# Optimization experiments

Measured on AMD Instinct MI355X. Metric: run time of the kernel, lower is better.

The kernel has to match this reference:

```python
import jax, jax.numpy as jnp
import numpy as np

N_HID = 256
N_IN = 2
N_OUT = 2
BATCH = 256
LENGTH = 1024
ALPHA = 0.25
SIGMA_NEU = 0.05
N_CON = 6553


def setup_inputs() -> dict:
    key = jax.random.key(0)
    k1, k2, k3, k4, k5 = jax.random.split(key, 5)
    rng = np.random.RandomState(0)
    # masked recurrent weight pieces (match torch __init__ construction)
    w_0 = rng.randn(N_HID, N_HID) / np.sqrt(N_HID)
    abs_w_0 = jnp.asarray(np.abs(w_0), dtype=jnp.float32)
    is_con_np = np.zeros((N_HID, N_HID), dtype=np.float32)
    ind_in = rng.choice(np.arange(N_HID), size=N_CON)
    ind_out = rng.choice(np.arange(N_HID), size=N_CON)
    is_con_np[ind_in, ind_out] = 1.0
    w_sign = jnp.asarray(np.sign(rng.randn(N_HID, N_HID)), dtype=jnp.float32)
    is_con = jnp.asarray(is_con_np)
    return {
        "input_signal": jax.random.normal(k1, (BATCH, LENGTH, N_IN), dtype=jnp.float32),
        "hidden": jnp.zeros((BATCH, N_HID), dtype=jnp.float32),
        "w_in": jax.random.normal(k2, (N_HID, N_IN), dtype=jnp.float32) / np.sqrt(N_IN),
        "w_out": jax.random.normal(k3, (N_OUT, N_HID), dtype=jnp.float32) / np.sqrt(N_HID),
        "abs_w_0": abs_w_0,
        "w_sign": w_sign,
        "is_con": is_con,
    }


def reference(input_signal, hidden, w_in, w_out, abs_w_0, w_sign, is_con):
    # masked signed recurrent weight: theta = |w0| * mask; w_hh = sign * theta where mask>0
    theta = abs_w_0 * is_con
    w_hh = jnp.where(is_con > 0, w_sign * theta, jnp.zeros_like(theta))  # [H,H]

    alpha = jnp.full((N_HID,), ALPHA, dtype=input_signal.dtype)
    x = jnp.transpose(input_signal, (1, 0, 2))  # [T,B,I]
    # input projection for all timesteps at once (w_in has no bias)
    inp_proj = jnp.einsum("tbi,hi->tbh", x, w_in)  # [T,B,H]
    # iid per-step neural noise: randn * sigma * sqrt(alpha)
    noise = (jax.random.normal(jax.random.key(42), (LENGTH, BATCH, N_HID), dtype=input_signal.dtype)
             * SIGMA_NEU * jnp.sqrt(alpha))

    def step(h, uv):
        u, n = uv
        tmp = u + jnp.tanh(h) @ w_hh.T  # F.linear(tanh(h), w_hh)
        h_new = (1.0 - alpha) * h + alpha * tmp + n
        return h_new, h_new

    h_last, hs = jax.lax.scan(step, hidden, (inp_proj, noise))  # hs: [T,B,H]
    outputs = jnp.einsum("tbh,oh->tbo", hs, w_out)  # [T,B,O]
    hidden_list = jnp.transpose(hs, (1, 0, 2))  # [B,T,H]
    output_list = jnp.transpose(outputs, (1, 0, 2))  # [B,T,O]
    return hidden_list, output_list, h_last
```

## Files before the change

### kernel.cpp

```cpp
#include <hip/hip_runtime.h>
#include <stdint.h>

#define TT 1024
#define HB 256
#define NE 48
#define NE2 24
#define O1 67108864u
#define O2 (67108864u + 524288u)

__device__ __forceinline__ uint32_t rotl32(uint32_t x, uint32_t r){ return (x<<r)|(x>>(32u-r)); }

#define RND(r) { x0+=x1; x1=rotl32(x1,(r)); x1^=x0; }
__device__ __forceinline__ void tf2x32(uint32_t k0,uint32_t k1,uint32_t& x0,uint32_t& x1){
  const uint32_t ks2 = 0x1BD11BDAu ^ k0 ^ k1;
  x0 += k0; x1 += k1;
  RND(13) RND(15) RND(26) RND(6)  x0+=k1;  x1+=ks2+1u;
  RND(17) RND(29) RND(16) RND(24) x0+=ks2; x1+=k0+2u;
  RND(13) RND(15) RND(26) RND(6)  x0+=k0;  x1+=k1+3u;
  RND(17) RND(29) RND(16) RND(24) x0+=k1;  x1+=ks2+4u;
  RND(13) RND(15) RND(26) RND(6)  x0+=ks2; x1+=k0+5u;
}
#undef RND

__device__ __forceinline__ float bits_to_noise(uint32_t bits){
  float f = __uint_as_float((bits>>9) | 0x3F800000u) - 1.0f;
  const float lo = -0.99999994f;
  float x = fmaxf(fmaf(f, 1.99999994f, lo), lo);
  float m = (1.0f - x) * (1.0f + x);
  float w = -0.69314718056f * __log2f(m);
  float p;
  if (w < 5.0f){
    w -= 2.5f;
    p = 2.81022636e-08f;
    p = fmaf(p, w, 3.43273939e-07f);
    p = fmaf(p, w, -3.5233877e-06f);
    p = fmaf(p, w, -4.39150654e-06f);
    p = fmaf(p, w, 0.00021858087f);
    p = fmaf(p, w, -0.00125372503f);
    p = fmaf(p, w, -0.00417768164f);
    p = fmaf(p, w, 0.246640727f);
    p = fmaf(p, w, 1.50140941f);
  } else {
    w = __fsqrt_rn(w) - 3.0f;
    p = -0.000200214257f;
    p = fmaf(p, w, 0.000100950558f);
    p = fmaf(p, w, 0.00134934322f);
    p = fmaf(p, w, -0.00367342844f);
    p = fmaf(p, w, 0.00573950773f);
    p = fmaf(p, w, -0.0076224613f);
    p = fmaf(p, w, 0.00943887047f);
    p = fmaf(p, w, 1.00167406f);
    p = fmaf(p, w, 2.83297682f);
  }
  return 0.035355339059f * (p * x);
}

__global__ void init_flags(uint32_t* flags){
  if (flags) { flags[0]=0u; flags[1]=0u; }
}

__global__ void check_kernel(float* out, const uint32_t* flags){
  uint32_t a0=0u, a1=0u;                 tf2x32(0u,0u,a0,a1);
  uint32_t b0=0xffffffffu, b1=0xffffffffu; tf2x32(0xffffffffu,0xffffffffu,b0,b1);
  uint32_t c0=0x243f6a88u, c1=0x85a308d3u; tf2x32(0x13198a2eu,0x03707344u,c0,c1);
  if (!(a0==0x6b200159u && a1==0x99ba4efeu)) out[0] = 1e30f;
  if (!(b0==0x1cb996fcu && b1==0xbb002be7u)) out[1] = 2e30f;
  if (!(c0==0xc4923a9cu && c1==0x483df7a0u)) out[2] = 3e30f;
  if (flags && flags[0]) out[5] = 6e30f;
}

__launch_bounds__(1024)
__global__ void rnn_kernel(const float* __restrict__ input_signal,
                           const float* __restrict__ hidden0,
                           const float* __restrict__ w_in,
                           const float* __restrict__ w_out,
                           const float* __restrict__ abs_w0,
                           const float* __restrict__ w_sign,
                           const float* __restrict__ is_con,
                           float* __restrict__ out,
                           uint32_t* __restrict__ flags)
{
  __shared__ float    ew[HB][NE];
  __shared__ uint16_t ei[HB][NE];
  __shared__ float    xbuf[TT*2];
  __shared__ float    hstage[8][HB];
  __shared__ float    nbuf[4][HB];
  __shared__ float    tbuf[2][HB];
  __shared__ int      cnts[HB];
  __shared__ int      rankinv[HB];
  __shared__ int      rof4[HB];
  __shared__ float    wot0[HB], wot1[HB];

  const int tid = threadIdx.x;
  const int b   = blockIdx.x;
  const bool gw = (tid < 512);

  {
    const float* xg = input_signal + (uint64_t)b*TT*2;
    *(float2*)(xbuf + tid*2) = *(const float2*)(xg + tid*2);
  }
  if (tid < HB){
    int c = 0;
    const float* ic = is_con + tid*HB;
    for (int k = 0; k < HB; k += 4){
      float4 c4 = *(const float4*)(ic + k);
      c += (c4.x>0.f)+(c4.y>0.f)+(c4.z>0.f)+(c4.w>0.f);
    }
    cnts[tid] = c;
    if (c > NE && flags) flags[0] = 1u;
  }
  __syncthreads();

  if (tid < HB){
    int myc = cnts[tid], r = 0;
    for (int k = 0; k < HB; ++k){
      int ck = cnts[k];
      r += (int)((ck > myc) || (ck == myc && k < tid));
    }
    rankinv[r] = tid;
    rof4[tid]  = r << 2;
  }
  __syncthreads();

  uint32_t bj = 0u;
  if (tid < HB){
    const int j = tid;
    const float* ic = is_con + j*HB;
    const float* aw = abs_w0 + j*HB;
    const float* ws = w_sign + j*HB;
    int n = 0;
    for (int k = 0; k < HB; ++k){
      if (ic[k] > 0.f && n < NE){
        ew[j][n] = ws[k]*aw[k];
        ei[j][n] = (uint16_t)rof4[k];
        ++n;
      }
    }
    for (int s = n; s < NE; ++s){ ew[j][s] = 0.f; ei[j][s] = (uint16_t)rof4[j]; }
    wot0[rof4[j]>>2] = w_out[j];
    wot1[rof4[j]>>2] = w_out[HB + j];
  } else if (tid >= 512){
    int m = tid - 512, rn = m >> 1, qn = m & 1;
    bj = (uint32_t)b*256u + (uint32_t)rankinv[rn];
    if (qn == 0){
      uint32_t x0 = 0u, x1 = bj;
      tf2x32(0u, 42u, x0, x1);
      nbuf[0][rn] = bits_to_noise(x0 ^ x1);
    }
  }
  __syncthreads();

  float    pwv[NE2];
  uint32_t piv[NE2/2];
  int trip = 0, row = 0, q = 0, rr = 0;
  float h = 0.f, wi0 = 0.f, wi1 = 0.f;
  float4 wo0 = {0,0,0,0}, wo1 = {0,0,0,0};
  int rf0 = 0, rf1 = 0;
  {
    int j0 = (tid & 127) << 1;
    rf0 = rof4[j0]; rf1 = rof4[j0+1];
  }
  if (gw){
    rr = tid >> 1; q = tid & 1;
    row = rankinv[rr];
    int c = cnts[row]; if (c > NE) c = NE;
    uint16_t pad = (uint16_t)rof4[row];
    uint32_t cur = 0u;
    #pragma unroll
    for (int s = 0; s < NE2; ++s){
      int idx = 2*s + q;
      float w = 0.f; uint32_t o = pad;
      if (idx < c){ w = ew[row][idx]; o = ei[row][idx]; }
      pwv[s] = w;
      if (s & 1) piv[s>>1] = cur | (o << 16); else cur = o;
    }
    trip = __builtin_amdgcn_readfirstlane((c + 1) >> 1);
    if (q == 0){
      h   = hidden0[b*HB + row];
      wi0 = w_in[row*2]; wi1 = w_in[row*2 + 1];
      tbuf[0][rr] = 1.0f - 2.0f/(__expf(2.0f*h) + 1.0f);
    }
  } else {
    int m = tid - 512;
    if (m < 128){
      int lam = m & 63;
      wo0 = *(const float4*)(wot0 + lam*4);
      wo1 = *(const float4*)(wot1 + lam*4);
    }
  }
  float* hrow = out + (uint64_t)b*TT*HB;
  float* orow = out + O1 + (uint64_t)b*TT*2;
  __syncthreads();

  for (int t = 0; t < TT; ++t){
    const int par = t & 1;
    if (gw){
      const char* tb = (const char*)(&tbuf[par][0]);
      float y0 = 0.f, y1 = 0.f;
      #pragma unroll
      for (int s = 0; s < NE2; s += 2){
        if (s < trip){
          uint32_t pa = piv[s>>1];
          float t0 = *(const float*)(tb + (pa & 0xFFFFu));
          float t1 = *(const float*)(tb + (pa >> 16));
          y0 = fmaf(pwv[s],   t0, y0);
          y1 = fmaf(pwv[s+1], t1, y1);
        }
      }
      float y = y0 + y1;
      y += __shfl_xor(y, 1, 64);
      if (q == 0){
        float nz = nbuf[t&3][rr];
        float2 xv = *(const float2*)(xbuf + t*2);
        float u  = fmaf(xv.x, wi0, xv.y*wi1);
        h = fmaf(0.25f, u + y, 0.75f*h) + nz;
        hstage[t&7][rr] = h;
        tbuf[par^1][rr] = 1.0f - 2.0f/(__expf(2.0f*h) + 1.0f);
      }
    } else {
      int m = tid - 512;
      if (!(t & 1)){
        int tv = t + 1 + (m & 1);
        if (tv < TT){
          uint32_t x0 = 0u, x1 = (uint32_t)tv*65536u + bj;
          tf2x32(0u, 42u, x0, x1);
          nbuf[tv&3][m>>1] = bits_to_noise(x0 ^ x1);
        }
      } else if (m < 128){
        int tau = t - 2 + (m >> 6);
        if (tau >= 0){
          int lam = m & 63;
          float4 hv = *(const float4*)(&hstage[tau&7][lam*4]);
          float p0 = hv.x*wo0.x + hv.y*wo0.y + hv.z*wo0.z + hv.w*wo0.w;
          float p1 = hv.x*wo1.x + hv.y*wo1.y + hv.z*wo1.z + hv.w*wo1.w;
          #pragma unroll
          for (int d = 1; d < 64; d <<= 1){
            p0 += __shfl_xor(p0, d, 64);
            p1 += __shfl_xor(p1, d, 64);
          }
          if (lam == 0) *(float2*)(orow + tau*2) = make_float2(p0, p1);
        }
      }
    }
    __syncthreads();

    if ((t & 7) == 7){
      int s  = tid >> 7;
      int j0 = (tid & 127) << 1;
      const char* hs = (const char*)(&hstage[s][0]);
      float2 v;
      v.x = *(const float*)(hs + rf0);
      v.y = *(const float*)(hs + rf1);
      *(float2*)(hrow + (uint64_t)(t - 7 + s)*HB + j0) = v;
      __syncthreads();
    }
  }

  if (!gw){
    int m = tid - 512;
    if (m < 64){
      float4 hv = *(const float4*)(&hstage[7][m*4]);
      float p0 = hv.x*wo0.x + hv.y*wo0.y + hv.z*wo0.z + hv.w*wo0.w;
      float p1 = hv.x*wo1.x + hv.y*wo1.y + hv.z*wo1.z + hv.w*wo1.w;
      #pragma unroll
      for (int d = 1; d < 64; d <<= 1){
        p0 += __shfl_xor(p0, d, 64);
        p1 += __shfl_xor(p1, d, 64);
      }
      if (m == 0) *(float2*)(orow + (TT-1)*2) = make_float2(p0, p1);
    }
  }
  if (gw && q == 0) out[O2 + b*HB + row] = h;
}

extern "C" void kernel_launch(void* const* d_in, const int* in_sizes, int n_in,
                              void* d_out, int out_size, void* d_ws, size_t ws_size,
                              hipStream_t stream) {
  const float* input_signal = (const float*)d_in[0];
  const float* hidden       = (const float*)d_in[1];
  const float* w_in         = (const float*)d_in[2];
  const float* w_out        = (const float*)d_in[3];
  const float* abs_w0       = (const float*)d_in[4];
  const float* w_sign       = (const float*)d_in[5];
  const float* is_con       = (const float*)d_in[6];
  float* out = (float*)d_out;
  uint32_t* flags = (ws_size >= 8) ? (uint32_t*)d_ws : nullptr;

  init_flags<<<1, 1, 0, stream>>>(flags);
  rnn_kernel<<<256, 1024, 0, stream>>>(input_signal, hidden, w_in, w_out,
                                       abs_w0, w_sign, is_con, out, flags);
  check_kernel<<<1, 1, 0, stream>>>(out, flags);
}
```

Baseline: 893.4 us.

## Split Threefry noise across steps, double hstage ring, drop extra barrier

The noise generator is split into two halves (first three round groups and last two), computed on alternating steps by paired helper threads, so the per-step noise work is spread evenly rather than bunched on even steps. The hstage ring grows from 8 to 16 slots, so the hidden-state writeback lags by 8 steps and no longer needs its own __syncthreads; the last 8 rows are flushed after the loop. The compute waves also raise their scheduling priority and load all tanh operands before the FMA chain. The cost is more shared memory and a more involved indexing scheme, and a self-check is added for the split RNG.

```diff
diff --git a/kernel.cpp b/kernel.cpp
--- a/kernel.cpp
+++ b/kernel.cpp
@@ -11,15 +11,22 @@
 __device__ __forceinline__ uint32_t rotl32(uint32_t x, uint32_t r){ return (x<<r)|(x>>(32u-r)); }
 
 #define RND(r) { x0+=x1; x1=rotl32(x1,(r)); x1^=x0; }
-__device__ __forceinline__ void tf2x32(uint32_t k0,uint32_t k1,uint32_t& x0,uint32_t& x1){
-  const uint32_t ks2 = 0x1BD11BDAu ^ k0 ^ k1;
+__device__ __forceinline__ void tf_h1g(uint32_t k0,uint32_t k1,uint32_t ks2,uint32_t& x0,uint32_t& x1){
   x0 += k0; x1 += k1;
   RND(13) RND(15) RND(26) RND(6)  x0+=k1;  x1+=ks2+1u;
   RND(17) RND(29) RND(16) RND(24) x0+=ks2; x1+=k0+2u;
   RND(13) RND(15) RND(26) RND(6)  x0+=k0;  x1+=k1+3u;
+}
+__device__ __forceinline__ void tf_h2g(uint32_t k0,uint32_t k1,uint32_t ks2,uint32_t& x0,uint32_t& x1){
   RND(17) RND(29) RND(16) RND(24) x0+=k1;  x1+=ks2+4u;
   RND(13) RND(15) RND(26) RND(6)  x0+=ks2; x1+=k0+5u;
 }
+__device__ __forceinline__ void tf2x32(uint32_t k0,uint32_t k1,uint32_t& x0,uint32_t& x1){
+  const uint32_t ks2 = 0x1BD11BDAu ^ k0 ^ k1;
+  tf_h1g(k0,k1,ks2,x0,x1); tf_h2g(k0,k1,ks2,x0,x1);
+}
+__device__ __forceinline__ void tf_h1(uint32_t& x0, uint32_t& x1){ tf_h1g(0u,42u,0x1BD11BF0u,x0,x1); }
+__device__ __forceinline__ void tf_h2(uint32_t& x0, uint32_t& x1){ tf_h2g(0u,42u,0x1BD11BF0u,x0,x1); }
 #undef RND
 
 __device__ __forceinline__ float bits_to_noise(uint32_t bits){
@@ -66,6 +73,9 @@
   if (!(a0==0x6b200159u && a1==0x99ba4efeu)) out[0] = 1e30f;
   if (!(b0==0x1cb996fcu && b1==0xbb002be7u)) out[1] = 2e30f;
   if (!(c0==0xc4923a9cu && c1==0x483df7a0u)) out[2] = 3e30f;
+  uint32_t d0=7u, d1=9u; tf_h1(d0,d1); tf_h2(d0,d1);
+  uint32_t e0=7u, e1=9u; tf2x32(0u,42u,e0,e1);
+  if (!(d0==e0 && d1==e1)) out[3] = 4e30f;
   if (flags && flags[0]) out[5] = 6e30f;
 }
 
@@ -83,7 +93,7 @@
   __shared__ float    ew[HB][NE];
   __shared__ uint16_t ei[HB][NE];
   __shared__ float    xbuf[TT*2];
-  __shared__ float    hstage[8][HB];
+  __shared__ float    hstage[16][HB];
   __shared__ float    nbuf[4][HB];
   __shared__ float    tbuf[2][HB];
   __shared__ int      cnts[HB];
@@ -122,7 +132,7 @@
   }
   __syncthreads();
 
-  uint32_t bj = 0u;
+  uint32_t bj = 0u, ax0 = 0u, ax1 = 0u;
   if (tid < HB){
     const int j = tid;
     const float* ic = is_con + j*HB;
@@ -140,12 +150,15 @@
     wot0[rof4[j]>>2] = w_out[j];
     wot1[rof4[j]>>2] = w_out[HB + j];
   } else if (tid >= 512){
-    int m = tid - 512, rn = m >> 1, qn = m & 1;
+    int m2 = tid - 512, rn = m2 >> 1, qn = m2 & 1;
     bj = (uint32_t)b*256u + (uint32_t)rankinv[rn];
     if (qn == 0){
       uint32_t x0 = 0u, x1 = bj;
       tf2x32(0u, 42u, x0, x1);
       nbuf[0][rn] = bits_to_noise(x0 ^ x1);
+    } else {
+      ax0 = 0u; ax1 = 65536u + bj;
+      tf_h1(ax0, ax1);
     }
   }
   __syncthreads();
@@ -181,9 +194,9 @@
       tbuf[0][rr] = 1.0f - 2.0f/(__expf(2.0f*h) + 1.0f);
     }
   } else {
-    int m = tid - 512;
-    if (m < 128){
-      int lam = m & 63;
+    int m2 = tid - 512;
+    if (m2 < 128){
+      int lam = m2 & 63;
       wo0 = *(const float4*)(wot0 + lam*4);
       wo1 = *(const float4*)(wot1 + lam*4);
     }
@@ -195,16 +208,23 @@
   for (int t = 0; t < TT; ++t){
     const int par = t & 1;
     if (gw){
+      __builtin_amdgcn_s_setprio(1);
       const char* tb = (const char*)(&tbuf[par][0]);
+      float tv[NE2];
+      #pragma unroll
+      for (int s = 0; s < NE2; s += 2){
+        if (s < trip){
+          uint32_t pa = piv[s>>1];
+          tv[s]   = *(const float*)(tb + (pa & 0xFFFFu));
+          tv[s+1] = *(const float*)(tb + (pa >> 16));
+        }
+      }
       float y0 = 0.f, y1 = 0.f;
       #pragma unroll
       for (int s = 0; s < NE2; s += 2){
         if (s < trip){
-          uint32_t pa = piv[s>>1];
-          float t0 = *(const float*)(tb + (pa & 0xFFFFu));
-          float t1 = *(const float*)(tb + (pa >> 16));
-          y0 = fmaf(pwv[s],   t0, y0);
-          y1 = fmaf(pwv[s+1], t1, y1);
+          y0 = fmaf(pwv[s],   tv[s],   y0);
+          y1 = fmaf(pwv[s+1], tv[s+1], y1);
         }
       }
       float y = y0 + y1;
@@ -214,23 +234,29 @@
         float2 xv = *(const float2*)(xbuf + t*2);
         float u  = fmaf(xv.x, wi0, xv.y*wi1);
         h = fmaf(0.25f, u + y, 0.75f*h) + nz;
-        hstage[t&7][rr] = h;
+        hstage[t&15][rr] = h;
         tbuf[par^1][rr] = 1.0f - 2.0f/(__expf(2.0f*h) + 1.0f);
       }
+      __builtin_amdgcn_s_setprio(0);
     } else {
-      int m = tid - 512;
-      if (!(t & 1)){
-        int tv = t + 1 + (m & 1);
-        if (tv < TT){
-          uint32_t x0 = 0u, x1 = (uint32_t)tv*65536u + bj;
-          tf2x32(0u, 42u, x0, x1);
-          nbuf[tv&3][m>>1] = bits_to_noise(x0 ^ x1);
-        }
-      } else if (m < 128){
-        int tau = t - 2 + (m >> 6);
+      int m2 = tid - 512, rn = m2 >> 1, qn = m2 & 1;
+      if (((t+1) & 1) == qn){
+        if (t + 1 < TT){
+          uint32_t f0 = ax0, f1 = ax1;
+          tf_h2(f0, f1);
+          nbuf[(t+1)&3][rn] = bits_to_noise(f0 ^ f1);
+        }
+      } else {
+        if (t + 2 < TT){
+          ax0 = 0u; ax1 = (uint32_t)(t+2)*65536u + bj;
+          tf_h1(ax0, ax1);
+        }
+      }
+      if (m2 < 128 && (t & 1)){
+        int tau = t - 2 + (m2 >> 6);
         if (tau >= 0){
-          int lam = m & 63;
-          float4 hv = *(const float4*)(&hstage[tau&7][lam*4]);
+          int lam = m2 & 63;
+          float4 hv = *(const float4*)(&hstage[tau&15][lam*4]);
           float p0 = hv.x*wo0.x + hv.y*wo0.y + hv.z*wo0.z + hv.w*wo0.w;
           float p1 = hv.x*wo1.x + hv.y*wo1.y + hv.z*wo1.z + hv.w*wo1.w;
           #pragma unroll
@@ -244,22 +270,31 @@
     }
     __syncthreads();
 
-    if ((t & 7) == 7){
+    if ((t & 7) == 7 && t >= 15){
       int s  = tid >> 7;
       int j0 = (tid & 127) << 1;
-      const char* hs = (const char*)(&hstage[s][0]);
+      int rbase = t - 15;
+      const char* hs = (const char*)(&hstage[(rbase + s)&15][0]);
       float2 v;
       v.x = *(const float*)(hs + rf0);
       v.y = *(const float*)(hs + rf1);
-      *(float2*)(hrow + (uint64_t)(t - 7 + s)*HB + j0) = v;
-      __syncthreads();
-    }
-  }
-
+      *(float2*)(hrow + (uint64_t)(rbase + s)*HB + j0) = v;
+    }
+  }
+
+  {
+    int s  = tid >> 7;
+    int j0 = (tid & 127) << 1;
+    const char* hs = (const char*)(&hstage[(1016 + s)&15][0]);
+    float2 v;
+    v.x = *(const float*)(hs + rf0);
+    v.y = *(const float*)(hs + rf1);
+    *(float2*)(hrow + (uint64_t)(1016 + s)*HB + j0) = v;
+  }
   if (!gw){
-    int m = tid - 512;
-    if (m < 64){
-      float4 hv = *(const float4*)(&hstage[7][m*4]);
+    int m2 = tid - 512;
+    if (m2 < 64){
+      float4 hv = *(const float4*)(&hstage[1023&15][m2*4]);
       float p0 = hv.x*wo0.x + hv.y*wo0.y + hv.z*wo0.z + hv.w*wo0.w;
       float p1 = hv.x*wo1.x + hv.y*wo1.y + hv.z*wo1.z + hv.w*wo1.w;
       #pragma unroll
@@ -267,7 +302,7 @@
         p0 += __shfl_xor(p0, d, 64);
         p1 += __shfl_xor(p1, d, 64);
       }
-      if (m == 0) *(float2*)(orow + (TT-1)*2) = make_float2(p0, p1);
+      if (m2 == 0) *(float2*)(orow + (TT-1)*2) = make_float2(p0, p1);
     }
   }
   if (gw && q == 0) out[O2 + b*HB + row] = h;
```

After: 929.1 us. 1.04x slower.

## Use all 1024 threads for recurrence and split noise generation across steps

Applied to the files above, without the earlier changes.

Removes the split between 512 compute threads and 512 helper threads. All threads now run the sparse recurrent dot product with four lanes per row, halving the per-lane serial FMA chain, and every lane recomputes h redundantly. The Threefry noise generation is split into four phases, one run per timestep and staggered across thread groups, so each step carries a small slice of RNG work. The output projection is folded into the batched hidden-state writeback, using a 16-deep staging ring and a cross-wave partial-sum buffer. The cost is RNG and epilogue work on every lane's critical path each step, plus an extra shuffle stage.

```diff
diff --git a/kernel.cpp b/kernel.cpp
--- a/kernel.cpp
+++ b/kernel.cpp
@@ -4,30 +4,44 @@
 #define TT 1024
 #define HB 256
 #define NE 48
-#define NE2 24
+#define NS 12
 #define O1 67108864u
 #define O2 (67108864u + 524288u)
 
 __device__ __forceinline__ uint32_t rotl32(uint32_t x, uint32_t r){ return (x<<r)|(x>>(32u-r)); }
 
-#define RND(r) { x0+=x1; x1=rotl32(x1,(r)); x1^=x0; }
-__device__ __forceinline__ void tf2x32(uint32_t k0,uint32_t k1,uint32_t& x0,uint32_t& x1){
+#define R4(a,b,c,d) { x0+=x1; x1=rotl32(x1,(a)); x1^=x0; x0+=x1; x1=rotl32(x1,(b)); x1^=x0; \
+                      x0+=x1; x1=rotl32(x1,(c)); x1^=x0; x0+=x1; x1=rotl32(x1,(d)); x1^=x0; }
+
+__device__ __forceinline__ void tfq0(uint32_t& x0, uint32_t& x1){
+  x0 += 0u; x1 += 42u;
+  R4(13,15,26,6)  x0 += 42u;         x1 += 0x1BD11BF0u + 1u;
+  R4(17,29,16,24) x0 += 0x1BD11BF0u; x1 += 2u;
+}
+__device__ __forceinline__ void tfq1(uint32_t& x0, uint32_t& x1){
+  R4(13,15,26,6)  x0 += 0u;          x1 += 45u;
+  R4(17,29,16,24) x0 += 42u;         x1 += 0x1BD11BF0u + 4u;
+}
+__device__ __forceinline__ void tfq2(uint32_t& x0, uint32_t& x1){
+  R4(13,15,26,6)  x0 += 0x1BD11BF0u; x1 += 5u;
+}
+__device__ __forceinline__ void tf2x32g(uint32_t k0,uint32_t k1,uint32_t& x0,uint32_t& x1){
   const uint32_t ks2 = 0x1BD11BDAu ^ k0 ^ k1;
   x0 += k0; x1 += k1;
-  RND(13) RND(15) RND(26) RND(6)  x0+=k1;  x1+=ks2+1u;
-  RND(17) RND(29) RND(16) RND(24) x0+=ks2; x1+=k0+2u;
-  RND(13) RND(15) RND(26) RND(6)  x0+=k0;  x1+=k1+3u;
-  RND(17) RND(29) RND(16) RND(24) x0+=k1;  x1+=ks2+4u;
-  RND(13) RND(15) RND(26) RND(6)  x0+=ks2; x1+=k0+5u;
-}
-#undef RND
-
-__device__ __forceinline__ float bits_to_noise(uint32_t bits){
+  R4(13,15,26,6)  x0+=k1;  x1+=ks2+1u;
+  R4(17,29,16,24) x0+=ks2; x1+=k0+2u;
+  R4(13,15,26,6)  x0+=k0;  x1+=k1+3u;
+  R4(17,29,16,24) x0+=k1;  x1+=ks2+4u;
+  R4(13,15,26,6)  x0+=ks2; x1+=k0+5u;
+}
+
+__device__ __forceinline__ void noise_fin1(uint32_t bits, float& x, float& w){
   float f = __uint_as_float((bits>>9) | 0x3F800000u) - 1.0f;
-  const float lo = -0.99999994f;
-  float x = fmaxf(fmaf(f, 1.99999994f, lo), lo);
+  x = fmaxf(fmaf(f, 1.99999994f, -0.99999994f), -0.99999994f);
   float m = (1.0f - x) * (1.0f + x);
-  float w = -0.69314718056f * __log2f(m);
+  w = -0.69314718056f * __log2f(m);
+}
+__device__ __forceinline__ float noise_fin2(float x, float w){
   float p;
   if (w < 5.0f){
     w -= 2.5f;
@@ -54,18 +68,27 @@
   }
   return 0.035355339059f * (p * x);
 }
+__device__ __forceinline__ float noise_full(uint32_t v, uint32_t bjn){
+  uint32_t x0 = 0u, x1 = v*65536u + bjn;
+  tfq0(x0,x1); tfq1(x0,x1); tfq2(x0,x1);
+  float fx, fw; noise_fin1(x0^x1, fx, fw);
+  return noise_fin2(fx, fw);
+}
 
 __global__ void init_flags(uint32_t* flags){
   if (flags) { flags[0]=0u; flags[1]=0u; }
 }
 
 __global__ void check_kernel(float* out, const uint32_t* flags){
-  uint32_t a0=0u, a1=0u;                 tf2x32(0u,0u,a0,a1);
-  uint32_t b0=0xffffffffu, b1=0xffffffffu; tf2x32(0xffffffffu,0xffffffffu,b0,b1);
-  uint32_t c0=0x243f6a88u, c1=0x85a308d3u; tf2x32(0x13198a2eu,0x03707344u,c0,c1);
+  uint32_t a0=0u, a1=0u;                 tf2x32g(0u,0u,a0,a1);
+  uint32_t b0=0xffffffffu, b1=0xffffffffu; tf2x32g(0xffffffffu,0xffffffffu,b0,b1);
+  uint32_t c0=0x243f6a88u, c1=0x85a308d3u; tf2x32g(0x13198a2eu,0x03707344u,c0,c1);
   if (!(a0==0x6b200159u && a1==0x99ba4efeu)) out[0] = 1e30f;
   if (!(b0==0x1cb996fcu && b1==0xbb002be7u)) out[1] = 2e30f;
   if (!(c0==0xc4923a9cu && c1==0x483df7a0u)) out[2] = 3e30f;
+  uint32_t d0=7u, d1=9u; tfq0(d0,d1); tfq1(d0,d1); tfq2(d0,d1);
+  uint32_t e0=7u, e1=9u; tf2x32g(0u,42u,e0,e1);
+  if (!(d0==e0 && d1==e1)) out[3] = 4e30f;
   if (flags && flags[0]) out[5] = 6e30f;
 }
 
@@ -83,17 +106,16 @@
   __shared__ float    ew[HB][NE];
   __shared__ uint16_t ei[HB][NE];
   __shared__ float    xbuf[TT*2];
-  __shared__ float    hstage[8][HB];
+  __shared__ float    hstage[16][HB];
   __shared__ float    nbuf[4][HB];
   __shared__ float    tbuf[2][HB];
+  __shared__ float    opart[8][2][2];
   __shared__ int      cnts[HB];
   __shared__ int      rankinv[HB];
   __shared__ int      rof4[HB];
-  __shared__ float    wot0[HB], wot1[HB];
 
   const int tid = threadIdx.x;
   const int b   = blockIdx.x;
-  const bool gw = (tid < 512);
 
   {
     const float* xg = input_signal + (uint64_t)b*TT*2;
@@ -122,7 +144,11 @@
   }
   __syncthreads();
 
-  uint32_t bj = 0u;
+  const int rj  = tid & 255;
+  const int sub = tid >> 8;
+  uint32_t bjn = 0u, ax0 = 0u, ax1 = 0u;
+  float fx = 0.f, fw = 0.f;
+  bjn = (uint32_t)b*256u + (uint32_t)rankinv[rj];
   if (tid < HB){
     const int j = tid;
     const float* ic = is_con + j*HB;
@@ -137,140 +163,141 @@
       }
     }
     for (int s = n; s < NE; ++s){ ew[j][s] = 0.f; ei[j][s] = (uint16_t)rof4[j]; }
-    wot0[rof4[j]>>2] = w_out[j];
-    wot1[rof4[j]>>2] = w_out[HB + j];
-  } else if (tid >= 512){
-    int m = tid - 512, rn = m >> 1, qn = m & 1;
-    bj = (uint32_t)b*256u + (uint32_t)rankinv[rn];
-    if (qn == 0){
-      uint32_t x0 = 0u, x1 = bj;
-      tf2x32(0u, 42u, x0, x1);
-      nbuf[0][rn] = bits_to_noise(x0 ^ x1);
-    }
-  }
-  __syncthreads();
-
-  float    pwv[NE2];
-  uint32_t piv[NE2/2];
-  int trip = 0, row = 0, q = 0, rr = 0;
-  float h = 0.f, wi0 = 0.f, wi1 = 0.f;
-  float4 wo0 = {0,0,0,0}, wo1 = {0,0,0,0};
-  int rf0 = 0, rf1 = 0;
+  }
+  nbuf[sub][rj] = noise_full((uint32_t)sub, bjn);
+  __syncthreads();
+
+  const int rr = tid >> 2, q = tid & 3;
+  const int row = rankinv[rr];
+  float    pwv[NS];
+  uint32_t piv[NS/2];
+  int trip;
   {
-    int j0 = (tid & 127) << 1;
-    rf0 = rof4[j0]; rf1 = rof4[j0+1];
-  }
-  if (gw){
-    rr = tid >> 1; q = tid & 1;
-    row = rankinv[rr];
     int c = cnts[row]; if (c > NE) c = NE;
-    uint16_t pad = (uint16_t)rof4[row];
-    uint32_t cur = 0u;
+    uint32_t pad = (uint32_t)rof4[row];
     #pragma unroll
-    for (int s = 0; s < NE2; ++s){
-      int idx = 2*s + q;
+    for (int s = 0; s < NS; ++s){
+      int idx = 4*s + q;
       float w = 0.f; uint32_t o = pad;
       if (idx < c){ w = ew[row][idx]; o = ei[row][idx]; }
       pwv[s] = w;
-      if (s & 1) piv[s>>1] = cur | (o << 16); else cur = o;
-    }
-    trip = __builtin_amdgcn_readfirstlane((c + 1) >> 1);
-    if (q == 0){
-      h   = hidden0[b*HB + row];
-      wi0 = w_in[row*2]; wi1 = w_in[row*2 + 1];
-      tbuf[0][rr] = 1.0f - 2.0f/(__expf(2.0f*h) + 1.0f);
-    }
-  } else {
-    int m = tid - 512;
-    if (m < 128){
-      int lam = m & 63;
-      wo0 = *(const float4*)(wot0 + lam*4);
-      wo1 = *(const float4*)(wot1 + lam*4);
-    }
-  }
+      if (s & 1) piv[s>>1] |= (o << 16); else piv[s>>1] = o;
+    }
+    trip = __builtin_amdgcn_readfirstlane((c + 3) >> 2);
+  }
+  float h   = hidden0[b*HB + row];
+  const float wi0 = w_in[row*2], wi1 = w_in[row*2 + 1];
+  const int j0 = (tid & 127) << 1;
+  const int rf0 = rof4[j0], rf1 = rof4[j0+1];
+  const float wo00 = w_out[j0],      wo01 = w_out[j0+1];
+  const float wo10 = w_out[HB + j0], wo11 = w_out[HB + j0 + 1];
+  if (q == 0) tbuf[0][rr] = 1.0f - 2.0f/(__expf(2.0f*h) + 1.0f);
   float* hrow = out + (uint64_t)b*TT*HB;
   float* orow = out + O1 + (uint64_t)b*TT*2;
   __syncthreads();
 
   for (int t = 0; t < TT; ++t){
     const int par = t & 1;
-    if (gw){
-      const char* tb = (const char*)(&tbuf[par][0]);
+
+    if (t >= sub){
+      int i = (t - sub) & 3;
+      if (i == 0){
+        ax0 = 0u; ax1 = (uint32_t)(t+4)*65536u + bjn;
+        tfq0(ax0, ax1);
+      } else if (i == 1){
+        tfq1(ax0, ax1);
+      } else if (i == 2){
+        tfq2(ax0, ax1);
+        noise_fin1(ax0 ^ ax1, fx, fw);
+      } else {
+        nbuf[(t+1)&3][rj] = noise_fin2(fx, fw);
+      }
+    }
+
+    {
+      const char* tb = (const char*)(&tbuf[0][0]) + par*1024;
       float y0 = 0.f, y1 = 0.f;
       #pragma unroll
-      for (int s = 0; s < NE2; s += 2){
+      for (int s = 0; s < NS; s += 2){
         if (s < trip){
           uint32_t pa = piv[s>>1];
-          float t0 = *(const float*)(tb + (pa & 0xFFFFu));
-          float t1 = *(const float*)(tb + (pa >> 16));
-          y0 = fmaf(pwv[s],   t0, y0);
-          y1 = fmaf(pwv[s+1], t1, y1);
+          y0 = fmaf(pwv[s],   *(const float*)(tb + (pa & 0xFFFFu)), y0);
+          y1 = fmaf(pwv[s+1], *(const float*)(tb + (pa >> 16)),     y1);
         }
       }
       float y = y0 + y1;
       y += __shfl_xor(y, 1, 64);
+      y += __shfl_xor(y, 2, 64);
+      float nz = nbuf[t&3][rr];
+      float2 xv = *(const float2*)(xbuf + t*2);
+      float u = fmaf(xv.x, wi0, xv.y*wi1);
+      h = fmaf(0.25f, u + y, 0.75f*h) + nz;
       if (q == 0){
-        float nz = nbuf[t&3][rr];
-        float2 xv = *(const float2*)(xbuf + t*2);
-        float u  = fmaf(xv.x, wi0, xv.y*wi1);
-        h = fmaf(0.25f, u + y, 0.75f*h) + nz;
-        hstage[t&7][rr] = h;
+        hstage[t&15][rr] = h;
         tbuf[par^1][rr] = 1.0f - 2.0f/(__expf(2.0f*h) + 1.0f);
       }
-    } else {
-      int m = tid - 512;
-      if (!(t & 1)){
-        int tv = t + 1 + (m & 1);
-        if (tv < TT){
-          uint32_t x0 = 0u, x1 = (uint32_t)tv*65536u + bj;
-          tf2x32(0u, 42u, x0, x1);
-          nbuf[tv&3][m>>1] = bits_to_noise(x0 ^ x1);
-        }
-      } else if (m < 128){
-        int tau = t - 2 + (m >> 6);
-        if (tau >= 0){
-          int lam = m & 63;
-          float4 hv = *(const float4*)(&hstage[tau&7][lam*4]);
-          float p0 = hv.x*wo0.x + hv.y*wo0.y + hv.z*wo0.z + hv.w*wo0.w;
-          float p1 = hv.x*wo1.x + hv.y*wo1.y + hv.z*wo1.z + hv.w*wo1.w;
-          #pragma unroll
-          for (int d = 1; d < 64; d <<= 1){
-            p0 += __shfl_xor(p0, d, 64);
-            p1 += __shfl_xor(p1, d, 64);
-          }
-          if (lam == 0) *(float2*)(orow + tau*2) = make_float2(p0, p1);
-        }
-      }
     }
     __syncthreads();
 
-    if ((t & 7) == 7){
-      int s  = tid >> 7;
-      int j0 = (tid & 127) << 1;
-      const char* hs = (const char*)(&hstage[s][0]);
+    if ((t & 7) == 0 && t >= 16 && tid < 16){
+      int s = tid >> 1, o = tid & 1;
+      orow[(t - 16 + s)*2 + o] = opart[s][0][o] + opart[s][1][o];
+    }
+    if ((t & 7) == 7 && t >= 15){
+      int s = tid >> 7;
+      int rbase = t - 15;
+      const char* hs = (const char*)(&hstage[(rbase + s)&15][0]);
       float2 v;
       v.x = *(const float*)(hs + rf0);
       v.y = *(const float*)(hs + rf1);
-      *(float2*)(hrow + (uint64_t)(t - 7 + s)*HB + j0) = v;
-      __syncthreads();
-    }
-  }
-
-  if (!gw){
-    int m = tid - 512;
-    if (m < 64){
-      float4 hv = *(const float4*)(&hstage[7][m*4]);
-      float p0 = hv.x*wo0.x + hv.y*wo0.y + hv.z*wo0.z + hv.w*wo0.w;
-      float p1 = hv.x*wo1.x + hv.y*wo1.y + hv.z*wo1.z + hv.w*wo1.w;
+      *(float2*)(hrow + (uint64_t)(rbase + s)*HB + j0) = v;
+      float p0 = fmaf(v.x, wo00, v.y*wo01);
+      float p1 = fmaf(v.x, wo10, v.y*wo11);
       #pragma unroll
       for (int d = 1; d < 64; d <<= 1){
         p0 += __shfl_xor(p0, d, 64);
         p1 += __shfl_xor(p1, d, 64);
       }
-      if (m == 0) *(float2*)(orow + (TT-1)*2) = make_float2(p0, p1);
-    }
-  }
-  if (gw && q == 0) out[O2 + b*HB + row] = h;
+      if ((tid & 63) == 0){
+        int w2 = (tid >> 6) & 1;
+        opart[s][w2][0] = p0;
+        opart[s][w2][1] = p1;
+      }
+    }
+  }
+
+  __syncthreads();
+  if (tid < 16){
+    int s = tid >> 1, o = tid & 1;
+    orow[(1008 + s)*2 + o] = opart[s][0][o] + opart[s][1][o];
+  }
+  __syncthreads();
+  {
+    int s = tid >> 7;
+    const char* hs = (const char*)(&hstage[(1016 + s)&15][0]);
+    float2 v;
+    v.x = *(const float*)(hs + rf0);
+    v.y = *(const float*)(hs + rf1);
+    *(float2*)(hrow + (uint64_t)(1016 + s)*HB + j0) = v;
+    float p0 = fmaf(v.x, wo00, v.y*wo01);
+    float p1 = fmaf(v.x, wo10, v.y*wo11);
+    #pragma unroll
+    for (int d = 1; d < 64; d <<= 1){
+      p0 += __shfl_xor(p0, d, 64);
+      p1 += __shfl_xor(p1, d, 64);
+    }
+    if ((tid & 63) == 0){
+      int w2 = (tid >> 6) & 1;
+      opart[s][w2][0] = p0;
+      opart[s][w2][1] = p1;
+    }
+  }
+  __syncthreads();
+  if (tid < 16){
+    int s = tid >> 1, o = tid & 1;
+    orow[(1016 + s)*2 + o] = opart[s][0][o] + opart[s][1][o];
+  }
+  if (q == 0) out[O2 + b*HB + row] = h;
 }
 
 extern "C" void kernel_launch(void* const* d_in, const int* in_sizes, int n_in,
```

Result: slower. 1.067 ms (+19.4%).
